# Optimization experiments

Measured on AMD Instinct MI355X. Metric: run time of the kernel, lower is better.

Reference implementation:

```python
import jax, jax.numpy as jnp
import numpy as np
import math

S, B, D, H = 2048, 4, 1024, 16
DH = D // H

def setup_inputs() -> dict:
    key = jax.random.key(0)
    ks = jax.random.split(key, 6)
    x = jax.random.normal(ks[0], (S, B, D), dtype=jnp.float32)
    # causal additive mask (finite large negative for numerical safety)
    i = jnp.arange(S)
    attn_mask = jnp.where(i[None, :] > i[:, None], jnp.float32(-1e9), jnp.float32(0.0))
    beta = jnp.zeros((H,), dtype=jnp.float32)  # per-head log-scale, init 0 -> exp=1
    xav = math.sqrt(6.0 / (D + D))  # xavier_uniform bound
    Wq = jax.random.uniform(ks[1], (D, D), minval=-xav, maxval=xav, dtype=jnp.float32)
    Wk = jax.random.uniform(ks[2], (D, D), minval=-xav, maxval=xav, dtype=jnp.float32)
    Wv = jax.random.uniform(ks[3], (D, D), minval=-xav, maxval=xav, dtype=jnp.float32)
    Wo = jax.random.uniform(ks[4], (D, D), minval=-xav, maxval=xav, dtype=jnp.float32)
    z = jnp.zeros((D,), dtype=jnp.float32)
    return {"x": x, "attn_mask": attn_mask, "beta": beta,
            "Wq": Wq, "bq": z, "Wk": Wk, "bk": z, "Wv": Wv, "bv": z, "Wo": Wo, "bo": z}

def reference(x, attn_mask, beta, Wq, bq, Wk, bk, Wv, bv, Wo, bo):
    s, b, d = x.shape
    h, dh = H, DH
    q = x @ Wq.T + bq  # (s, b, d)
    k = x @ Wk.T + bk
    v = x @ Wv.T + bv
    # attn_sink: append zero key/value token, pad mask with a zero column
    k = jnp.concatenate([k, jnp.zeros((1, b, d), k.dtype)], axis=0)  # (s+1, b, d)
    v = jnp.concatenate([v, jnp.zeros((1, b, d), v.dtype)], axis=0)
    mask = jnp.pad(attn_mask, ((0, 0), (0, 1)))  # (s, s+1)
    t = s + 1
    # split heads: (seq, b, h, dh) -> (b, h, seq, dh)
    qh = q.reshape(s, b, h, dh).transpose(1, 2, 0, 3)
    kh = k.reshape(t, b, h, dh).transpose(1, 2, 0, 3)
    vh = v.reshape(t, b, h, dh).transpose(1, 2, 0, 3)
    scale = (jnp.exp(beta) * math.sqrt(dh))[None, :, None, None]
    qh = qh / scale
    scores = jnp.einsum('bhsd,bhtd->bhst', qh, kh) + mask[None, None]
    w = jax.nn.softmax(scores, axis=-1)
    out = jnp.einsum('bhst,bhtd->bhsd', w, vh)  # (b, h, s, dh)
    out = out.transpose(2, 0, 1, 3).reshape(s, b, d)
    return out @ Wo.T + bo
```

## Files before the change

kernel.cpp:

```cpp
#include <hip/hip_runtime.h>
#include <hip/hip_bf16.h>
#include <math.h>

#define S_LEN   2048
#define BATCH   4
#define DMODEL  1024
#define NHEAD   16
#define DHEAD   64
#define MROWS   (S_LEN * BATCH)

typedef __bf16 bf16;
typedef __bf16 bf16x8 __attribute__((ext_vector_type(8)));
typedef __bf16 bf16x4 __attribute__((ext_vector_type(4)));
typedef short  short4_t __attribute__((ext_vector_type(4)));
typedef float  f32x4  __attribute__((ext_vector_type(4)));

#define LOG2E 1.4426950408889634f

#define AS1C(p) (const __attribute__((address_space(1))) void*)(p)
#define AS3(p)  (__attribute__((address_space(3))) void*)(p)


__global__ __launch_bounds__(256) void cast_all(const float* __restrict__ x,
                                                const float* __restrict__ wq,
                                                const float* __restrict__ wk,
                                                const float* __restrict__ wv,
                                                const float* __restrict__ wo,
                                                bf16* __restrict__ xb,
                                                bf16* __restrict__ wqkv,
                                                bf16* __restrict__ wob) {
    const int i = blockIdx.x * 256 + threadIdx.x;
    constexpr int NX8 = MROWS * DMODEL / 8;
    constexpr int NW8 = DMODEL * DMODEL / 8;
    const float* src;
    bf16* dst;
    int k;
    if (i < NX8) {
        src = x; dst = xb; k = i;
    } else {
        const int j   = i - NX8;
        const int seg = j >> 17;
        k = j & (NW8 - 1);
        if (seg == 0)      { src = wq; dst = wqkv; }
        else if (seg == 1) { src = wk; dst = wqkv + (size_t)DMODEL * DMODEL; }
        else if (seg == 2) { src = wv; dst = wqkv + (size_t)2 * DMODEL * DMODEL; }
        else               { src = wo; dst = wob; }
    }
    const float4* p = (const float4*)src;
    float4 a = p[(size_t)k * 2], b = p[(size_t)k * 2 + 1];
    bf16x8 o;
    o[0] = (bf16)a.x; o[1] = (bf16)a.y; o[2] = (bf16)a.z; o[3] = (bf16)a.w;
    o[4] = (bf16)b.x; o[5] = (bf16)b.y; o[6] = (bf16)b.z; o[7] = (bf16)b.w;
    *(bf16x8*)(dst + (size_t)k * 8) = o;
}

__global__ __launch_bounds__(512, 6) void qkv_gemm(const bf16* __restrict__ A,
                                                   const bf16* __restrict__ W,
                                                   const float* __restrict__ bq,
                                                   const float* __restrict__ bk,
                                                   const float* __restrict__ bv,
                                                   const float* __restrict__ beta,
                                                   bf16* __restrict__ Qo,
                                                   bf16* __restrict__ Kp,
                                                   bf16* __restrict__ Vp) {
    constexpr int BK = 32;
    constexpr int NT = DMODEL / BK;
    __shared__ __align__(16) bf16 sA[3][128 * BK];
    __shared__ __align__(16) bf16 sB[3][128 * BK];
    const int t    = threadIdx.x;
    const int lane = t & 63;
    const int wave = t >> 6;
    const int wr   = wave >> 2;
    const int wc   = wave & 3;
    const int lq   = lane & 15;
    const int lg   = lane >> 4;
    const int bn   = blockIdx.x * 128;
    const int bm   = blockIdx.y * 128;

    const int schunk = (lane & 3) ^ ((lane >> 3) & 3);
    const bf16* ApS = A + (size_t)(bm + wave * 16 + (lane >> 2)) * DMODEL + schunk * 8;
    const bf16* WpS = W + (size_t)(bn + wave * 16 + (lane >> 2)) * DMODEL + schunk * 8;
    const int koff = (lg ^ ((lq >> 1) & 3)) * 8;
    f32x4 acc[4][2] = {};

#define QSTG(si_, ko_)                                                                   \
    __builtin_amdgcn_global_load_lds(AS1C(ApS + (ko_)), AS3(&sA[si_][wave * 512]), 16, 0, 0); \
    __builtin_amdgcn_global_load_lds(AS1C(WpS + (ko_)), AS3(&sB[si_][wave * 512]), 16, 0, 0);

    QSTG(0, 0)
    QSTG(1, BK)
    asm volatile("s_waitcnt vmcnt(2)\n\ts_barrier" ::: "memory");

    int bi = 0, si = 2, st = 2;
    for (int tt = 0; tt < NT; ++tt) {
        QSTG(si, (size_t)st * BK)
        const bf16* At = sA[bi];
        const bf16* Bt = sB[bi];
        bf16x8 bf0 = *(const bf16x8*)&Bt[(wc * 32 +      lq) * BK + koff];
        bf16x8 bf1 = *(const bf16x8*)&Bt[(wc * 32 + 16 + lq) * BK + koff];
        bf16x8 af[4];
#pragma unroll
        for (int mt = 0; mt < 4; mt++)
            af[mt] = *(const bf16x8*)&At[(wr * 64 + mt * 16 + lq) * BK + koff];
        __builtin_amdgcn_s_setprio(1);
#pragma unroll
        for (int mt = 0; mt < 4; mt++) {
            acc[mt][0] = __builtin_amdgcn_mfma_f32_16x16x32_bf16(af[mt], bf0, acc[mt][0], 0, 0, 0);
            acc[mt][1] = __builtin_amdgcn_mfma_f32_16x16x32_bf16(af[mt], bf1, acc[mt][1], 0, 0, 0);
        }
        __builtin_amdgcn_s_setprio(0);
        asm volatile("s_waitcnt vmcnt(2)\n\ts_barrier" ::: "memory");
        bi = (bi == 2) ? 0 : bi + 1;
        si = (si == 2) ? 0 : si + 1;
        st = (st == NT - 1) ? 0 : st + 1;
    }
#undef QSTG

    const int seg = blockIdx.x >> 3;
    const int bnl = (blockIdx.x & 7) * 128;
    const float* bias = (seg == 0) ? bq : (seg == 1) ? bk : bv;

    if (seg == 0) {
#pragma unroll
        for (int nt = 0; nt < 2; nt++) {
            const int col = bnl + wc * 32 + nt * 16 + lq;
            const float bvv = bias[col];
            const float sc = LOG2E / (__expf(beta[col >> 6]) * 8.0f);
#pragma unroll
            for (int mt = 0; mt < 4; mt++) {
                const int row = bm + wr * 64 + mt * 16 + lg * 4;
#pragma unroll
                for (int r = 0; r < 4; r++) {
                    float v = (acc[mt][nt][r] + bvv) * sc;
                    Qo[(size_t)(row + r) * DMODEL + col] = (bf16)v;
                }
            }
        }
    } else {
        bf16* out = (seg == 1) ? Kp : Vp;
#pragma unroll
        for (int mt = 0; mt < 4; mt++) {
            const int F   = bm + wr * 64 + mt * 16;
            const int S0X = F >> 2;
            const int T   = S0X >> 4;
            const int sl  = (S0X & 15) + lg;
#pragma unroll
            for (int nt = 0; nt < 2; nt++) {
                const int col = bnl + wc * 32 + nt * 16 + lq;
                const int h   = col >> 6;
                const int dh  = col & 63;
                const float bvv = bias[col];
#pragma unroll
                for (int r = 0; r < 4; r++) {
                    float v = acc[mt][nt][r] + bvv;
                    size_t addr;
                    if (seg == 1) {
                        addr = ((size_t)((r * 16 + h) * 128 + T)) * 1024
                             + (dh >> 5) * 512
                             + (sl + 16 * ((dh >> 3) & 3)) * 8
                             + (dh & 7);
                    } else {
                        addr = ((size_t)((r * 16 + h) * 128 + T)) * 1024
                             + (dh >> 4) * 256 + ((dh & 15) + 16 * (sl >> 2)) * 4
                             + (sl & 3);
                    }
                    out[addr] = (bf16)v;
                }
            }
        }
    }
}

__global__ __launch_bounds__(256, 3) void gemm_out(const bf16* __restrict__ A,
                                                   const bf16* __restrict__ W,
                                                   const float* __restrict__ bias,
                                                   float* __restrict__ C) {
    constexpr int BK = 32;
    constexpr int NTILES = DMODEL / BK;
    __shared__ __align__(16) bf16 sA[3][128 * BK];
    __shared__ __align__(16) bf16 sB[3][128 * BK];

    const int t    = threadIdx.x;
    const int lane = t & 63;
    const int wave = t >> 6;
    const int wr   = wave >> 1;
    const int wc   = wave & 1;
    const int lq   = lane & 15;
    const int lg   = lane >> 4;
    const int bn   = blockIdx.x * 128;
    const int bm   = blockIdx.y * 128;

    const int schunk = (lane & 3) ^ ((lane >> 3) & 3);
    const bf16* ApS = A + (size_t)(bm + wave * 32 + (lane >> 2)) * DMODEL + schunk * 8;
    const bf16* WpS = W + (size_t)(bn + wave * 32 + (lane >> 2)) * DMODEL + schunk * 8;
    const int koff = (lg ^ ((lq >> 1) & 3)) * 8;

    f32x4 acc[4][4] = {};

#define OSTAGE(si_, ko_)                                                                              \
    __builtin_amdgcn_global_load_lds(AS1C(ApS + (ko_)),               AS3(&sA[si_][(wave*32 +  0)*BK]), 16,0,0); \
    __builtin_amdgcn_global_load_lds(AS1C(ApS + 16*DMODEL + (ko_)),   AS3(&sA[si_][(wave*32 + 16)*BK]), 16,0,0); \
    __builtin_amdgcn_global_load_lds(AS1C(WpS + (ko_)),               AS3(&sB[si_][(wave*32 +  0)*BK]), 16,0,0); \
    __builtin_amdgcn_global_load_lds(AS1C(WpS + 16*DMODEL + (ko_)),   AS3(&sB[si_][(wave*32 + 16)*BK]), 16,0,0);

    OSTAGE(0, 0)
    OSTAGE(1, BK)
    asm volatile("s_waitcnt vmcnt(4)\n\ts_barrier" ::: "memory");

    int bi = 0, si = 2, st = 2;
    for (int tt = 0; tt < NTILES; ++tt) {
        OSTAGE(si, (size_t)st * BK)
        const bf16* At = sA[bi];
        const bf16* Bt = sB[bi];
        bf16x8 bfr[4], af[4];
#pragma unroll
        for (int nt = 0; nt < 4; nt++)
            bfr[nt] = *(const bf16x8*)&Bt[(wc * 64 + nt * 16 + lq) * BK + koff];
#pragma unroll
        for (int mt = 0; mt < 4; mt++)
            af[mt] = *(const bf16x8*)&At[(wr * 64 + mt * 16 + lq) * BK + koff];
        __builtin_amdgcn_s_setprio(1);
#pragma unroll
        for (int mt = 0; mt < 4; mt++)
#pragma unroll
            for (int nt = 0; nt < 4; nt++)
                acc[mt][nt] = __builtin_amdgcn_mfma_f32_16x16x32_bf16(af[mt], bfr[nt], acc[mt][nt], 0, 0, 0);
        __builtin_amdgcn_s_setprio(0);
        asm volatile("s_waitcnt vmcnt(4)\n\ts_barrier" ::: "memory");
        bi = (bi == 2) ? 0 : bi + 1;
        si = (si == 2) ? 0 : si + 1;
        st = (st == NTILES - 1) ? 0 : st + 1;
    }
#undef OSTAGE

#pragma unroll
    for (int nt = 0; nt < 4; nt++) {
        const int col = bn + wc * 64 + nt * 16 + lq;
        const float bvv = bias[col];
#pragma unroll
        for (int mt = 0; mt < 4; mt++) {
            const int row = bm + wr * 64 + mt * 16 + lg * 4;
#pragma unroll
            for (int r = 0; r < 4; r++)
                C[(size_t)(row + r) * DMODEL + col] = acc[mt][nt][r] + bvv;
        }
    }
}

__global__ __launch_bounds__(256, 3) void attn_kernel(const bf16* __restrict__ Q,
                                                      const bf16* __restrict__ Kp,
                                                      const bf16* __restrict__ Vp,
                                                      bf16* __restrict__ O) {
    __shared__ __align__(16) float sO[64 * 65];
    __shared__ __align__(16) float sL[256];

    const int t    = threadIdx.x;
    const int lane = t & 63;
    const int wave = t >> 6;
    const int lq = lane & 15;
    const int lg = lane >> 4;

    const int bid = (int)blockIdx.x + 16 * ((int)blockIdx.y + 16 * (int)blockIdx.z);
    const int swz = (bid & 7) * 128 + (bid >> 3);
    const int idx = swz & 15;
    const int h   = (swz >> 4) & 15;
    const int b   = swz >> 8;

    const bf16* Kb = Kp + (size_t)(b * NHEAD + h) * 131072;
    const bf16* Vb = Vp + (size_t)(b * NHEAD + h) * 131072;

#pragma clang loop unroll(disable)
    for (int pass = 0; pass < 2; ++pass) {
        const int qi = (pass == 0) ? (31 - idx) : idx;
        const int qb = qi * 64;

        bf16x8 qf[4][2];
#pragma unroll
        for (int nt = 0; nt < 4; nt++)
#pragma unroll
            for (int kc = 0; kc < 2; kc++)
                qf[nt][kc] = *(const bf16x8*)
                    &Q[((size_t)(qb + nt * 16 + lq) * BATCH + b) * DMODEL + h * DHEAD + kc * 32 + lg * 8];

        f32x4 o_acc[4][4] = {};
        float l_lane[4] = {0.f, 0.f, 0.f, 0.f};

        bf16x8 kc0 = *(const bf16x8*)(Kb + (size_t)wave * 1024 + lane * 8);
        bf16x8 kc1 = *(const bf16x8*)(Kb + (size_t)wave * 1024 + 512 + lane * 8);
        bf16x4 vc0 = *(const bf16x4*)(Vb + (size_t)wave * 1024 +   0 + lane * 4);
        bf16x4 vc1 = *(const bf16x4*)(Vb + (size_t)wave * 1024 + 256 + lane * 4);
        bf16x4 vc2 = *(const bf16x4*)(Vb + (size_t)wave * 1024 + 512 + lane * 4);
        bf16x4 vc3 = *(const bf16x4*)(Vb + (size_t)wave * 1024 + 768 + lane * 4);

        for (int kt = 0; kt <= qi; kt++) {
            const int tn = ((kt < qi) ? (kt + 1) : 0) * 4 + wave;
            const bf16* Kn = Kb + (size_t)tn * 1024;
            const bf16* Vn = Vb + (size_t)tn * 1024;
            bf16x8 kn0 = *(const bf16x8*)(Kn + lane * 8);
            bf16x8 kn1 = *(const bf16x8*)(Kn + 512 + lane * 8);
            bf16x4 vn0 = *(const bf16x4*)(Vn +   0 + lane * 4);
            bf16x4 vn1 = *(const bf16x4*)(Vn + 256 + lane * 4);
            bf16x4 vn2 = *(const bf16x4*)(Vn + 512 + lane * 4);
            bf16x4 vn3 = *(const bf16x4*)(Vn + 768 + lane * 4);

            f32x4 st[4];
            __builtin_amdgcn_s_setprio(1);
#pragma unroll
            for (int nt = 0; nt < 4; nt++) {
                f32x4 a = {};
                a = __builtin_amdgcn_mfma_f32_16x16x32_bf16(kc0, qf[nt][0], a, 0, 0, 0);
                a = __builtin_amdgcn_mfma_f32_16x16x32_bf16(kc1, qf[nt][1], a, 0, 0, 0);
                st[nt] = a;
            }
            __builtin_amdgcn_s_setprio(0);

            if (kt == qi) {
#pragma unroll
                for (int nt = 0; nt < 4; nt++)
#pragma unroll
                    for (int r = 0; r < 4; r++)
                        if (wave * 16 + lg * 4 + r > nt * 16 + lq) st[nt][r] = -1e30f;
            }

            short4_t pf[4];
#pragma unroll
            for (int nt = 0; nt < 4; nt++) {
                float p0 = __builtin_amdgcn_exp2f(st[nt][0]);
                float p1 = __builtin_amdgcn_exp2f(st[nt][1]);
                float p2 = __builtin_amdgcn_exp2f(st[nt][2]);
                float p3 = __builtin_amdgcn_exp2f(st[nt][3]);
                l_lane[nt] += (p0 + p1) + (p2 + p3);
                bf16x4 pv;
                pv[0] = (bf16)p0; pv[1] = (bf16)p1; pv[2] = (bf16)p2; pv[3] = (bf16)p3;
                pf[nt] = __builtin_bit_cast(short4_t, pv);
            }

            short4_t va0 = __builtin_bit_cast(short4_t, vc0);
            short4_t va1 = __builtin_bit_cast(short4_t, vc1);
            short4_t va2 = __builtin_bit_cast(short4_t, vc2);
            short4_t va3 = __builtin_bit_cast(short4_t, vc3);
            __builtin_amdgcn_s_setprio(1);
#pragma unroll
            for (int nt = 0; nt < 4; nt++) {
                o_acc[0][nt] = __builtin_amdgcn_mfma_f32_16x16x16bf16_1k(va0, pf[nt], o_acc[0][nt], 0, 0, 0);
                o_acc[1][nt] = __builtin_amdgcn_mfma_f32_16x16x16bf16_1k(va1, pf[nt], o_acc[1][nt], 0, 0, 0);
                o_acc[2][nt] = __builtin_amdgcn_mfma_f32_16x16x16bf16_1k(va2, pf[nt], o_acc[2][nt], 0, 0, 0);
                o_acc[3][nt] = __builtin_amdgcn_mfma_f32_16x16x16bf16_1k(va3, pf[nt], o_acc[3][nt], 0, 0, 0);
            }
            __builtin_amdgcn_s_setprio(0);

            kc0 = kn0; kc1 = kn1;
            vc0 = vn0; vc1 = vn1; vc2 = vn2; vc3 = vn3;
        }

#pragma unroll
        for (int nt = 0; nt < 4; nt++) {
            float v = l_lane[nt];
            v += __shfl_xor(v, 16);
            v += __shfl_xor(v, 32);
            if (lg == 0) sL[wave * 64 + nt * 16 + lq] = v;
        }

#pragma unroll
        for (int rd = 0; rd < 4; rd++) {
#pragma unroll
            for (int dtc = 0; dtc < 4; dtc++) {
                if (((wave + rd) & 3) == dtc) {
                    if (rd == 0) {
#pragma unroll
                        for (int nt = 0; nt < 4; nt++)
#pragma unroll
                            for (int r = 0; r < 4; r++)
                                sO[(dtc * 16 + lg * 4 + r) * 65 + nt * 16 + lq] = o_acc[dtc][nt][r];
                    } else {
#pragma unroll
                        for (int nt = 0; nt < 4; nt++)
#pragma unroll
                            for (int r = 0; r < 4; r++)
                                sO[(dtc * 16 + lg * 4 + r) * 65 + nt * 16 + lq] += o_acc[dtc][nt][r];
                    }
                }
            }
            __syncthreads();
        }

        const int dt = wave;
        float rec[4];
#pragma unroll
        for (int nt = 0; nt < 4; nt++) {
            float lt = 1.0f + sL[nt * 16 + lq] + sL[64 + nt * 16 + lq]
                     + sL[128 + nt * 16 + lq] + sL[192 + nt * 16 + lq];
            rec[nt] = 1.0f / lt;
        }
#pragma unroll
        for (int nt = 0; nt < 4; nt++) {
            bf16x4 ov;
#pragma unroll
            for (int r = 0; r < 4; r++)
                ov[r] = (bf16)(sO[(dt * 16 + lg * 4 + r) * 65 + nt * 16 + lq] * rec[nt]);
            *(bf16x4*)&O[((size_t)(qb + nt * 16 + lq) * BATCH + b) * DMODEL + h * DHEAD + dt * 16 + lg * 4] = ov;
        }

        __syncthreads();
    }
}

extern "C" void kernel_launch(void* const* d_in, const int* in_sizes, int n_in,
                              void* d_out, int out_size, void* d_ws, size_t ws_size,
                              hipStream_t stream) {
    const float* x    = (const float*)d_in[0];
    const float* beta = (const float*)d_in[2];
    const float* Wq   = (const float*)d_in[3];
    const float* bq   = (const float*)d_in[4];
    const float* Wk   = (const float*)d_in[5];
    const float* bk   = (const float*)d_in[6];
    const float* Wv   = (const float*)d_in[7];
    const float* bv   = (const float*)d_in[8];
    const float* Wo   = (const float*)d_in[9];
    const float* bo   = (const float*)d_in[10];
    float* out = (float*)d_out;

    char* ws = (char*)d_ws;
    size_t off = 0;
    auto alloc = [&](size_t bytes) -> void* {
        void* p = ws + off;
        off += (bytes + 255) & ~(size_t)255;
        return p;
    };
    const size_t xbytes = (size_t)MROWS * DMODEL * sizeof(bf16);
    const size_t wbytes = (size_t)DMODEL * DMODEL * sizeof(bf16);
    bf16* xb   = (bf16*)alloc(xbytes);
    bf16* wqkv = (bf16*)alloc(3 * wbytes);
    bf16* wob  = (bf16*)alloc(wbytes);
    bf16* qws  = (bf16*)alloc(xbytes);
    bf16* kpb  = (bf16*)alloc(xbytes);
    bf16* vpb  = (bf16*)alloc(xbytes);
    bf16* aob  = (bf16*)alloc(xbytes);

    constexpr int NX8 = MROWS * DMODEL / 8;
    constexpr int NW8 = DMODEL * DMODEL / 8;
    cast_all<<<(NX8 + 4 * NW8) / 256, 256, 0, stream>>>(x, Wq, Wk, Wv, Wo, xb, wqkv, wob);

    dim3 qgrid(3 * DMODEL / 128, MROWS / 128);
    qkv_gemm<<<qgrid, 512, 0, stream>>>(xb, wqkv, bq, bk, bv, beta, qws, kpb, vpb);

    dim3 agrid(S_LEN / 128, NHEAD, BATCH);
    attn_kernel<<<agrid, 256, 0, stream>>>(qws, kpb, vpb, aob);

    dim3 ogrid(DMODEL / 128, MROWS / 128);
    gemm_out<<<ogrid, 256, 0, stream>>>(aob, wob, bo, out);
}
```

Measured before the change: 271.4 us.

## Split attention by query rows per wave, removing cross-wave LDS reduction

The attention kernel now gives each wave its own 16 query rows and has it loop over all key tiles up to the causal boundary. Previously the waves split keys and combined partial outputs through shared memory with several barriers. The two-pass pairing of short and long query blocks per workgroup is replaced by one query block per workgroup on a doubled grid, and the occupancy hint rises to 4. Each wave now reloads every K/V tile itself instead of sharing the key range across waves, which raises redundant global/L2 traffic. Work per wave also becomes uneven within a block, since waves stop at different tile counts.

After: 364.1 us. +34.1%, slower.

```diff
diff --git a/kernel.cpp b/kernel.cpp
--- a/kernel.cpp
+++ b/kernel.cpp
@@ -247,161 +247,103 @@
     }
 }
 
-__global__ __launch_bounds__(256, 3) void attn_kernel(const bf16* __restrict__ Q,
+__global__ __launch_bounds__(256, 4) void attn_kernel(const bf16* __restrict__ Q,
                                                       const bf16* __restrict__ Kp,
                                                       const bf16* __restrict__ Vp,
                                                       bf16* __restrict__ O) {
-    __shared__ __align__(16) float sO[64 * 65];
-    __shared__ __align__(16) float sL[256];
-
     const int t    = threadIdx.x;
     const int lane = t & 63;
     const int wave = t >> 6;
     const int lq = lane & 15;
     const int lg = lane >> 4;
 
-    const int bid = (int)blockIdx.x + 16 * ((int)blockIdx.y + 16 * (int)blockIdx.z);
-    const int swz = (bid & 7) * 128 + (bid >> 3);
-    const int idx = swz & 15;
-    const int h   = (swz >> 4) & 15;
-    const int b   = swz >> 8;
+    const int bid = (int)blockIdx.x + 32 * ((int)blockIdx.y + 16 * (int)blockIdx.z);
+    const int swz = (bid & 7) * 256 + (bid >> 3);
+    const int qi  = 31 - (swz & 31);
+    const int h   = (swz >> 5) & 15;
+    const int b   = swz >> 9;
+    const int qb  = qi * 64;
 
     const bf16* Kb = Kp + (size_t)(b * NHEAD + h) * 131072;
     const bf16* Vb = Vp + (size_t)(b * NHEAD + h) * 131072;
 
-#pragma clang loop unroll(disable)
-    for (int pass = 0; pass < 2; ++pass) {
-        const int qi = (pass == 0) ? (31 - idx) : idx;
-        const int qb = qi * 64;
-
-        bf16x8 qf[4][2];
-#pragma unroll
-        for (int nt = 0; nt < 4; nt++)
-#pragma unroll
-            for (int kc = 0; kc < 2; kc++)
-                qf[nt][kc] = *(const bf16x8*)
-                    &Q[((size_t)(qb + nt * 16 + lq) * BATCH + b) * DMODEL + h * DHEAD + kc * 32 + lg * 8];
-
-        f32x4 o_acc[4][4] = {};
-        float l_lane[4] = {0.f, 0.f, 0.f, 0.f};
-
-        bf16x8 kc0 = *(const bf16x8*)(Kb + (size_t)wave * 1024 + lane * 8);
-        bf16x8 kc1 = *(const bf16x8*)(Kb + (size_t)wave * 1024 + 512 + lane * 8);
-        bf16x4 vc0 = *(const bf16x4*)(Vb + (size_t)wave * 1024 +   0 + lane * 4);
-        bf16x4 vc1 = *(const bf16x4*)(Vb + (size_t)wave * 1024 + 256 + lane * 4);
-        bf16x4 vc2 = *(const bf16x4*)(Vb + (size_t)wave * 1024 + 512 + lane * 4);
-        bf16x4 vc3 = *(const bf16x4*)(Vb + (size_t)wave * 1024 + 768 + lane * 4);
-
-        for (int kt = 0; kt <= qi; kt++) {
-            const int tn = ((kt < qi) ? (kt + 1) : 0) * 4 + wave;
-            const bf16* Kn = Kb + (size_t)tn * 1024;
-            const bf16* Vn = Vb + (size_t)tn * 1024;
-            bf16x8 kn0 = *(const bf16x8*)(Kn + lane * 8);
-            bf16x8 kn1 = *(const bf16x8*)(Kn + 512 + lane * 8);
-            bf16x4 vn0 = *(const bf16x4*)(Vn +   0 + lane * 4);
-            bf16x4 vn1 = *(const bf16x4*)(Vn + 256 + lane * 4);
-            bf16x4 vn2 = *(const bf16x4*)(Vn + 512 + lane * 4);
-            bf16x4 vn3 = *(const bf16x4*)(Vn + 768 + lane * 4);
-
-            f32x4 st[4];
-            __builtin_amdgcn_s_setprio(1);
-#pragma unroll
-            for (int nt = 0; nt < 4; nt++) {
-                f32x4 a = {};
-                a = __builtin_amdgcn_mfma_f32_16x16x32_bf16(kc0, qf[nt][0], a, 0, 0, 0);
-                a = __builtin_amdgcn_mfma_f32_16x16x32_bf16(kc1, qf[nt][1], a, 0, 0, 0);
-                st[nt] = a;
-            }
-            __builtin_amdgcn_s_setprio(0);
-
-            if (kt == qi) {
-#pragma unroll
-                for (int nt = 0; nt < 4; nt++)
-#pragma unroll
-                    for (int r = 0; r < 4; r++)
-                        if (wave * 16 + lg * 4 + r > nt * 16 + lq) st[nt][r] = -1e30f;
-            }
-
-            short4_t pf[4];
-#pragma unroll
-            for (int nt = 0; nt < 4; nt++) {
-                float p0 = __builtin_amdgcn_exp2f(st[nt][0]);
-                float p1 = __builtin_amdgcn_exp2f(st[nt][1]);
-                float p2 = __builtin_amdgcn_exp2f(st[nt][2]);
-                float p3 = __builtin_amdgcn_exp2f(st[nt][3]);
-                l_lane[nt] += (p0 + p1) + (p2 + p3);
-                bf16x4 pv;
-                pv[0] = (bf16)p0; pv[1] = (bf16)p1; pv[2] = (bf16)p2; pv[3] = (bf16)p3;
-                pf[nt] = __builtin_bit_cast(short4_t, pv);
-            }
-
-            short4_t va0 = __builtin_bit_cast(short4_t, vc0);
-            short4_t va1 = __builtin_bit_cast(short4_t, vc1);
-            short4_t va2 = __builtin_bit_cast(short4_t, vc2);
-            short4_t va3 = __builtin_bit_cast(short4_t, vc3);
-            __builtin_amdgcn_s_setprio(1);
-#pragma unroll
-            for (int nt = 0; nt < 4; nt++) {
-                o_acc[0][nt] = __builtin_amdgcn_mfma_f32_16x16x16bf16_1k(va0, pf[nt], o_acc[0][nt], 0, 0, 0);
-                o_acc[1][nt] = __builtin_amdgcn_mfma_f32_16x16x16bf16_1k(va1, pf[nt], o_acc[1][nt], 0, 0, 0);
-                o_acc[2][nt] = __builtin_amdgcn_mfma_f32_16x16x16bf16_1k(va2, pf[nt], o_acc[2][nt], 0, 0, 0);
-                o_acc[3][nt] = __builtin_amdgcn_mfma_f32_16x16x16bf16_1k(va3, pf[nt], o_acc[3][nt], 0, 0, 0);
-            }
-            __builtin_amdgcn_s_setprio(0);
-
-            kc0 = kn0; kc1 = kn1;
-            vc0 = vn0; vc1 = vn1; vc2 = vn2; vc3 = vn3;
-        }
-
-#pragma unroll
-        for (int nt = 0; nt < 4; nt++) {
-            float v = l_lane[nt];
-            v += __shfl_xor(v, 16);
-            v += __shfl_xor(v, 32);
-            if (lg == 0) sL[wave * 64 + nt * 16 + lq] = v;
-        }
-
-#pragma unroll
-        for (int rd = 0; rd < 4; rd++) {
-#pragma unroll
-            for (int dtc = 0; dtc < 4; dtc++) {
-                if (((wave + rd) & 3) == dtc) {
-                    if (rd == 0) {
-#pragma unroll
-                        for (int nt = 0; nt < 4; nt++)
-#pragma unroll
-                            for (int r = 0; r < 4; r++)
-                                sO[(dtc * 16 + lg * 4 + r) * 65 + nt * 16 + lq] = o_acc[dtc][nt][r];
-                    } else {
-#pragma unroll
-                        for (int nt = 0; nt < 4; nt++)
-#pragma unroll
-                            for (int r = 0; r < 4; r++)
-                                sO[(dtc * 16 + lg * 4 + r) * 65 + nt * 16 + lq] += o_acc[dtc][nt][r];
-                    }
-                }
-            }
-            __syncthreads();
-        }
-
-        const int dt = wave;
-        float rec[4];
-#pragma unroll
-        for (int nt = 0; nt < 4; nt++) {
-            float lt = 1.0f + sL[nt * 16 + lq] + sL[64 + nt * 16 + lq]
-                     + sL[128 + nt * 16 + lq] + sL[192 + nt * 16 + lq];
-            rec[nt] = 1.0f / lt;
-        }
-#pragma unroll
-        for (int nt = 0; nt < 4; nt++) {
-            bf16x4 ov;
+    bf16x8 qf0 = *(const bf16x8*)
+        &Q[((size_t)(qb + wave * 16 + lq) * BATCH + b) * DMODEL + h * DHEAD +  0 + lg * 8];
+    bf16x8 qf1 = *(const bf16x8*)
+        &Q[((size_t)(qb + wave * 16 + lq) * BATCH + b) * DMODEL + h * DHEAD + 32 + lg * 8];
+
+    f32x4 o_acc[4] = {};
+    float l_lane = 0.f;
+
+    const int ntiles = qi * 4 + wave + 1;
+
+    bf16x8 kc0 = *(const bf16x8*)(Kb + lane * 8);
+    bf16x8 kc1 = *(const bf16x8*)(Kb + 512 + lane * 8);
+    bf16x4 vc0 = *(const bf16x4*)(Vb +   0 + lane * 4);
+    bf16x4 vc1 = *(const bf16x4*)(Vb + 256 + lane * 4);
+    bf16x4 vc2 = *(const bf16x4*)(Vb + 512 + lane * 4);
+    bf16x4 vc3 = *(const bf16x4*)(Vb + 768 + lane * 4);
+
+    for (int kt = 0; kt < ntiles; ++kt) {
+        const int tn = (kt + 1 < ntiles) ? (kt + 1) : 0;
+        const bf16* Kn = Kb + (size_t)tn * 1024;
+        const bf16* Vn = Vb + (size_t)tn * 1024;
+        bf16x8 kn0 = *(const bf16x8*)(Kn + lane * 8);
+        bf16x8 kn1 = *(const bf16x8*)(Kn + 512 + lane * 8);
+        bf16x4 vn0 = *(const bf16x4*)(Vn +   0 + lane * 4);
+        bf16x4 vn1 = *(const bf16x4*)(Vn + 256 + lane * 4);
+        bf16x4 vn2 = *(const bf16x4*)(Vn + 512 + lane * 4);
+        bf16x4 vn3 = *(const bf16x4*)(Vn + 768 + lane * 4);
+
+        f32x4 st = {};
+        __builtin_amdgcn_s_setprio(1);
+        st = __builtin_amdgcn_mfma_f32_16x16x32_bf16(kc0, qf0, st, 0, 0, 0);
+        st = __builtin_amdgcn_mfma_f32_16x16x32_bf16(kc1, qf1, st, 0, 0, 0);
+        __builtin_amdgcn_s_setprio(0);
+
+        if (kt == ntiles - 1) {
 #pragma unroll
             for (int r = 0; r < 4; r++)
-                ov[r] = (bf16)(sO[(dt * 16 + lg * 4 + r) * 65 + nt * 16 + lq] * rec[nt]);
-            *(bf16x4*)&O[((size_t)(qb + nt * 16 + lq) * BATCH + b) * DMODEL + h * DHEAD + dt * 16 + lg * 4] = ov;
-        }
-
-        __syncthreads();
+                if (lg * 4 + r > lq) st[r] = -1e30f;
+        }
+
+        float p0 = __builtin_amdgcn_exp2f(st[0]);
+        float p1 = __builtin_amdgcn_exp2f(st[1]);
+        float p2 = __builtin_amdgcn_exp2f(st[2]);
+        float p3 = __builtin_amdgcn_exp2f(st[3]);
+        l_lane += (p0 + p1) + (p2 + p3);
+        bf16x4 pv;
+        pv[0] = (bf16)p0; pv[1] = (bf16)p1; pv[2] = (bf16)p2; pv[3] = (bf16)p3;
+        short4_t pf = __builtin_bit_cast(short4_t, pv);
+
+        short4_t va0 = __builtin_bit_cast(short4_t, vc0);
+        short4_t va1 = __builtin_bit_cast(short4_t, vc1);
+        short4_t va2 = __builtin_bit_cast(short4_t, vc2);
+        short4_t va3 = __builtin_bit_cast(short4_t, vc3);
+        __builtin_amdgcn_s_setprio(1);
+        o_acc[0] = __builtin_amdgcn_mfma_f32_16x16x16bf16_1k(va0, pf, o_acc[0], 0, 0, 0);
+        o_acc[1] = __builtin_amdgcn_mfma_f32_16x16x16bf16_1k(va1, pf, o_acc[1], 0, 0, 0);
+        o_acc[2] = __builtin_amdgcn_mfma_f32_16x16x16bf16_1k(va2, pf, o_acc[2], 0, 0, 0);
+        o_acc[3] = __builtin_amdgcn_mfma_f32_16x16x16bf16_1k(va3, pf, o_acc[3], 0, 0, 0);
+        __builtin_amdgcn_s_setprio(0);
+
+        kc0 = kn0; kc1 = kn1;
+        vc0 = vn0; vc1 = vn1; vc2 = vn2; vc3 = vn3;
+    }
+
+    float lv = l_lane;
+    lv += __shfl_xor(lv, 16);
+    lv += __shfl_xor(lv, 32);
+    const float rec = 1.0f / (1.0f + lv);
+
+    const size_t orow = ((size_t)(qb + wave * 16 + lq) * BATCH + b) * DMODEL + h * DHEAD;
+#pragma unroll
+    for (int dt = 0; dt < 4; dt++) {
+        bf16x4 ov;
+#pragma unroll
+        for (int r = 0; r < 4; r++)
+            ov[r] = (bf16)(o_acc[dt][r] * rec);
+        *(bf16x4*)&O[orow + dt * 16 + lg * 4] = ov;
     }
 }
 
@@ -444,7 +386,7 @@
     dim3 qgrid(3 * DMODEL / 128, MROWS / 128);
     qkv_gemm<<<qgrid, 512, 0, stream>>>(xb, wqkv, bq, bk, bv, beta, qws, kpb, vpb);
 
-    dim3 agrid(S_LEN / 128, NHEAD, BATCH);
+    dim3 agrid(S_LEN / 64, NHEAD, BATCH);
     attn_kernel<<<agrid, 256, 0, stream>>>(qws, kpb, vpb, aob);
 
     dim3 ogrid(DMODEL / 128, MROWS / 128);
```
